# Optimization experiments

Hardware: AMD Instinct MI355X
Metric: run time of the kernel (lower is better)

Reference implementation:

```python
import jax, jax.numpy as jnp
import numpy as np

H = 4            # num_heads
D_HID = 128      # n_hidden (per head)
IN = 256         # in_feats
C = 47           # n_classes
NEG = 0.2        # DGL GATConv default negative_slope
NUM_SRC = (150000, 25000, 6000)
NUM_DST = (25000, 6000, 1024)
NUM_EDGES = (375000, 90000, 10240)


def gat_conv(h_src, h_dst, src, dst, Wsrc, Wdst, al, ar, b, num_dst, out_dim, apply_act):
    # h_src: [Ns, Fin], h_dst: [Nd, Fin]; Wsrc/Wdst: [H*out, Fin]; al/ar: [H, out]; b: [H*out]
    fs = (h_src @ Wsrc.T).reshape(-1, H, out_dim)          # [Ns,H,out]
    fd = (h_dst @ Wdst.T).reshape(-1, H, out_dim)          # [Nd,H,out]
    el = jnp.einsum('nhd,hd->nh', fs, al)                  # [Ns,H]
    er = jnp.einsum('nhd,hd->nh', fd, ar)                  # [Nd,H]
    e = jax.nn.leaky_relu(el[src] + er[dst], NEG)          # [E,H]
    # numerically-stable edge softmax per dst node
    m = jax.ops.segment_max(e, dst, num_segments=num_dst)  # [Nd,H]
    m = jnp.where(jnp.isfinite(m), m, 0.0)                 # guard isolated dst nodes
    ex = jnp.exp(e - m[dst])                               # [E,H]
    s = jax.ops.segment_sum(ex, dst, num_segments=num_dst) # [Nd,H]
    # weighted neighbor aggregation (scatter-add), normalize after the sum
    agg = jax.ops.segment_sum(ex[:, :, None] * fs[src], dst, num_segments=num_dst)  # [Nd,H,out]
    rst = agg / jnp.maximum(s, 1e-9)[:, :, None]
    rst = rst + b.reshape(1, H, out_dim)
    if apply_act:
        rst = jax.nn.elu(rst)
    return rst


def setup_inputs() -> dict:
    key = jax.random.key(0)
    ks = jax.random.split(key, 32)
    inp = {}
    inp['x'] = jax.random.normal(ks[0], (NUM_SRC[0], IN), dtype=jnp.float32)
    # sampled blocks as edge lists (dst nodes are prefix of src nodes)
    inp['src0'] = jax.random.randint(ks[1], (NUM_EDGES[0],), 0, NUM_SRC[0])
    inp['dst0'] = jax.random.randint(ks[2], (NUM_EDGES[0],), 0, NUM_DST[0])
    inp['src1'] = jax.random.randint(ks[3], (NUM_EDGES[1],), 0, NUM_SRC[1])
    inp['dst1'] = jax.random.randint(ks[4], (NUM_EDGES[1],), 0, NUM_DST[1])
    inp['src2'] = jax.random.randint(ks[5], (NUM_EDGES[2],), 0, NUM_SRC[2])
    inp['dst2'] = jax.random.randint(ks[6], (NUM_EDGES[2],), 0, NUM_DST[2])
    # layer params: (in_dim, out_per_head): (256,128), (512,128), (512,47)
    dims = [(IN, D_HID), (H * D_HID, D_HID), (H * D_HID, C)]
    k = 7
    for l, (fin, fout) in enumerate(dims):
        inp[f'Wsrc{l}'] = jax.random.normal(ks[k], (H * fout, fin), dtype=jnp.float32) * 0.05; k += 1
        inp[f'Wdst{l}'] = jax.random.normal(ks[k], (H * fout, fin), dtype=jnp.float32) * 0.05; k += 1
        inp[f'al{l}'] = jax.random.normal(ks[k], (H, fout), dtype=jnp.float32) * 0.05; k += 1
        inp[f'ar{l}'] = jax.random.normal(ks[k], (H, fout), dtype=jnp.float32) * 0.05; k += 1
        inp[f'b{l}'] = jnp.zeros((H * fout,), dtype=jnp.float32); k += 1
    return inp


def reference(x, src0, dst0, src1, dst1, src2, dst2,
              Wsrc0, Wdst0, al0, ar0, b0,
              Wsrc1, Wdst1, al1, ar1, b1,
              Wsrc2, Wdst2, al2, ar2, b2):
    h = x
    # layer 0
    h = gat_conv(h, h[:NUM_DST[0]], src0, dst0, Wsrc0, Wdst0, al0, ar0, b0,
                 NUM_DST[0], D_HID, True).reshape(NUM_DST[0], H * D_HID)
    # layer 1
    h = gat_conv(h, h[:NUM_DST[1]], src1, dst1, Wsrc1, Wdst1, al1, ar1, b1,
                 NUM_DST[1], D_HID, True).reshape(NUM_DST[1], H * D_HID)
    # layer 2 (no activation), mean over heads, log-softmax
    h = gat_conv(h, h[:NUM_DST[2]], src2, dst2, Wsrc2, Wdst2, al2, ar2, b2,
                 NUM_DST[2], C, False)                      # [1024,H,C]
    h = h.mean(axis=1)                                      # [1024,C]
    return jax.nn.log_softmax(h, axis=-1)
```

## Files before the change

kernel.cpp:

```cpp
#include <hip/hip_runtime.h>
#include <math.h>


#define E0 375000
#define E1 90000
#define E2 10240
#define ETOT (E0 + E1 + E2)
#define ND0 25000
#define ND1 6000
#define ND2 1024
#define NTOT (ND0 + ND1 + ND2)
#define NCH ((NTOT + 127) / 128)

static const int L_NS[3]   = {150000, 25000, 6000};
static const int L_ND[3]   = {ND0, ND1, ND2};

typedef short bf8_t __attribute__((ext_vector_type(8)));
typedef float f32x4 __attribute__((ext_vector_type(4)));

__device__ __forceinline__ float lrelu(float v) { return v >= 0.f ? v : 0.2f * v; }
__device__ __forceinline__ unsigned short f2b(float f) {
  unsigned u = __float_as_uint(f);
  unsigned r = u + 0x7fffu + ((u >> 16) & 1u);
  return (unsigned short)(r >> 16);
}
__device__ __forceinline__ float b2f(unsigned v) {
  return __uint_as_float(v << 16);
}
__device__ __forceinline__ unsigned bpack(float a, float b) {
  return (unsigned)f2b(a) | ((unsigned)f2b(b) << 16);
}

__device__ __forceinline__ void gload16(const unsigned short* g, unsigned short* l) {
  __builtin_amdgcn_global_load_lds(
      (const __attribute__((address_space(1))) unsigned int*)g,
      (__attribute__((address_space(3))) unsigned int*)l, 16, 0, 0);
}


__global__ void k_prep_count(
    const int* __restrict__ d0, const int* __restrict__ d1,
    const int* __restrict__ d2, int* __restrict__ cntAll, int* __restrict__ r,
    const float* __restrict__ Ws0, const float* __restrict__ Wd0,
    const float* __restrict__ al0, const float* __restrict__ ar0,
    const float* __restrict__ Ws1, const float* __restrict__ Wd1,
    const float* __restrict__ al1, const float* __restrict__ ar1,
    const float* __restrict__ Ws2, const float* __restrict__ Wd2,
    const float* __restrict__ al2, const float* __restrict__ ar2,
    unsigned short* __restrict__ wlrb, float* __restrict__ wlr1,
    float* __restrict__ wlr2,
    unsigned short* __restrict__ B0, unsigned short* __restrict__ B1,
    unsigned short* __restrict__ B2) {
  const int b = blockIdx.x, t = threadIdx.x;
  int gid = b * 256 + t;
  if (gid < ETOT) {
    int goff, dv;
    if (gid < E0) { goff = 0; dv = d0[gid]; }
    else if (gid < E0 + E1) { goff = ND0; dv = d1[gid - E0]; }
    else { goff = ND0 + ND1; dv = d2[gid - E0 - E1]; }
    r[gid] = atomicAdd(&cntAll[goff + dv], 1);
  }
  if (b < 8) {
    int h = b, hh = h & 3;
    const float* W = (h < 4) ? Ws0 : Wd0;
    const float* a = (h < 4) ? al0 : ar0;
    float acc = 0.f;
    for (int d = 0; d < 128; ++d)
      acc = fmaf(a[hh * 128 + d], W[(size_t)(hh * 128 + d) * 256 + t], acc);
    wlrb[h * 264 + t] = f2b(acc);
  } else if (b == 8) {
    for (int i = t; i < 8 * 264; i += 256) wlrb[8 * 264 + i] = 0;
  } else if (b < 17) {
    int idx = b - 9, which = idx >> 2, h = idx & 3;
    const float* W = which ? Wd1 : Ws1;
    const float* a = which ? ar1 : al1;
#pragma unroll
    for (int kc = 0; kc < 2; ++kc) {
      int k = kc * 256 + t;
      float acc = 0.f;
      for (int d = 0; d < 128; ++d)
        acc = fmaf(a[h * 128 + d], W[(size_t)(h * 128 + d) * 512 + k], acc);
      wlr1[which * 2048 + h * 512 + k] = acc;
    }
  } else if (b < 25) {
    int idx = b - 17, which = idx >> 2, h = idx & 3;
    const float* W = which ? Wd2 : Ws2;
    const float* a = which ? ar2 : al2;
#pragma unroll
    for (int kc = 0; kc < 2; ++kc) {
      int k = kc * 256 + t;
      float acc = 0.f;
      for (int d = 0; d < 47; ++d)
        acc = fmaf(a[h * 47 + d], W[(size_t)(h * 47 + d) * 512 + k], acc);
      wlr2[which * 2048 + h * 512 + k] = acc;
    }
  }
  const int n0 = 512 * 256, n1 = 512 * 512, n2 = 188 * 512;
  for (int i = gid; i < n0 + n1 + n2; i += gridDim.x * 256) {
    if (i < n0) B0[i] = f2b(Ws0[i]);
    else if (i < n0 + n1) B1[i - n0] = f2b(Ws1[i - n0]);
    else B2[i - n0 - n1] = f2b(Ws2[i - n0 - n1]);
  }
}

__global__ __launch_bounds__(128) void k_scanA(const int* __restrict__ cnt,
                                               int* __restrict__ S,
                                               int* __restrict__ btot, int n) {
  __shared__ int wt[2];
  int c = blockIdx.x, t = threadIdx.x, lane = t & 63, w = t >> 6;
  int g = c * 128 + t;
  int v = (g < n) ? cnt[g] : 0;
  int incl = v;
  for (int off = 1; off < 64; off <<= 1) {
    int u = __shfl_up(incl, off);
    if (lane >= off) incl += u;
  }
  if (lane == 63) wt[w] = incl;
  __syncthreads();
  int base = (w == 1) ? wt[0] : 0;
  if (g < n) S[g] = incl - v + base;
  if (t == 127) btot[c] = wt[0] + wt[1];
}

__global__ __launch_bounds__(256) void k_scanB(const int* __restrict__ btot,
                                               int* __restrict__ S, int n, int etot) {
  __shared__ int tv[256];
  int c = blockIdx.x, t = threadIdx.x;
  int own = (t < NCH) ? btot[t] : 0;
  tv[t] = own;
  __syncthreads();
  for (int off = 1; off < 256; off <<= 1) {
    int u = (t >= off) ? tv[t - off] : 0;
    __syncthreads();
    tv[t] += u;
    __syncthreads();
  }
  int base = tv[c] - btot[c];
  int g = c * 128 + (t & 127);
  if (t < 128 && g < n) S[g] += base;
  if (c == 0 && t == 255) S[n] = etot;
}

__global__ void k_scatter_all(
    const int* __restrict__ s0, const int* __restrict__ d0,
    const int* __restrict__ s1, const int* __restrict__ d1,
    const int* __restrict__ s2, const int* __restrict__ d2,
    const int* __restrict__ S, const int* __restrict__ r,
    int* __restrict__ cvAll) {
  int g = blockIdx.x * 256 + threadIdx.x;
  if (g >= ETOT) return;
  int goff, dv, sv;
  if (g < E0) { goff = 0; dv = d0[g]; sv = s0[g]; }
  else if (g < E0 + E1) { int e = g - E0; goff = ND0; dv = d1[e]; sv = s1[e]; }
  else { int e = g - E0 - E1; goff = ND0 + ND1; dv = d2[e]; sv = s2[e]; }
  cvAll[S[goff + dv] + r[g]] = sv;
}


__global__ __launch_bounds__(256) void k_dotc_mfma(
    const float* __restrict__ x, const unsigned short* __restrict__ wlrb,
    float* __restrict__ ell, float* __restrict__ err, int Ns, int Nd) {
  __shared__ unsigned short As[128 * 72];
  __shared__ unsigned short Bs[16 * 264];
  const int tid = threadIdx.x;
  const int w = tid >> 6, lane = tid & 63;
  const int bm = blockIdx.x * 128;
  const int rowg = tid >> 4;
  const int seg  = tid & 15;
  for (int i = tid; i < 16 * 264; i += 256) Bs[i] = wlrb[i];
  f32x4 acc[2] = {};
  for (int k0 = 0; k0 < 256; k0 += 64) {
    __syncthreads();
#pragma unroll
    for (int i = 0; i < 8; ++i) {
      int row = rowg + i * 16;
      int gm = bm + row;
      int gmc = gm < Ns ? gm : Ns - 1;
      float4 a = *reinterpret_cast<const float4*>(x + (size_t)gmc * 256 + k0 + seg * 4);
      ushort4 ub;
      ub.x = f2b(a.x); ub.y = f2b(a.y); ub.z = f2b(a.z); ub.w = f2b(a.w);
      *reinterpret_cast<ushort4*>(&As[row * 72 + seg * 4]) = ub;
    }
    __syncthreads();
    const int ra = w * 32 + (lane & 15);
    const int kf = (lane >> 4) * 8;
#pragma unroll
    for (int ks = 0; ks < 2; ++ks) {
      bf8_t b0 = *reinterpret_cast<const bf8_t*>(&Bs[(lane & 15) * 264 + k0 + ks * 32 + kf]);
      bf8_t a0 = *reinterpret_cast<const bf8_t*>(&As[ra * 72 + ks * 32 + kf]);
      bf8_t a1 = *reinterpret_cast<const bf8_t*>(&As[(ra + 16) * 72 + ks * 32 + kf]);
      acc[0] = __builtin_amdgcn_mfma_f32_16x16x32_bf16(a0, b0, acc[0], 0, 0, 0);
      acc[1] = __builtin_amdgcn_mfma_f32_16x16x32_bf16(a1, b0, acc[1], 0, 0, 0);
    }
  }
  int col = lane & 15;
#pragma unroll
  for (int fm = 0; fm < 2; ++fm) {
#pragma unroll
    for (int j = 0; j < 4; ++j) {
      int node = bm + w * 32 + fm * 16 + (lane >> 4) * 4 + j;
      if (node >= Ns) continue;
      float v = acc[fm][j];
      if (col < 4) ell[(size_t)node * 4 + col] = v;
      else if (col < 8 && node < Nd) err[(size_t)node * 4 + (col - 4)] = v;
    }
  }
}

__device__ __forceinline__ void reduce8_store(float v[8], int lane, int node, int Nd,
                                              float* __restrict__ ell,
                                              float* __restrict__ err) {
#pragma unroll
  for (int h = 0; h < 8; ++h) {
    v[h] += __shfl_xor(v[h], 8);
    v[h] += __shfl_xor(v[h], 16);
    v[h] += __shfl_xor(v[h], 32);
  }
  int sel = lane >> 3;
  float t01 = (sel & 1) ? v[1] : v[0];
  float t23 = (sel & 1) ? v[3] : v[2];
  float t45 = (sel & 1) ? v[5] : v[4];
  float t67 = (sel & 1) ? v[7] : v[6];
  float t03 = (sel & 2) ? t23 : t01;
  float t47 = (sel & 2) ? t67 : t45;
  float s   = (sel & 4) ? t47 : t03;
  s += __shfl_xor(s, 1);
  s += __shfl_xor(s, 2);
  s += __shfl_xor(s, 4);
  if ((lane & 7) == 0) {
    if (sel < 4) ell[(size_t)node * 4 + sel] = s;
    else if (node < Nd) err[(size_t)node * 4 + (sel - 4)] = s;
  }
}

__global__ __launch_bounds__(256) void k_dot_bf(
    const unsigned short* __restrict__ Hs, const float* __restrict__ wlr,
    float* __restrict__ ell, float* __restrict__ err, int Ns, int Nd) {
  int node = blockIdx.x * 4 + (threadIdx.x >> 6);
  int lane = threadIdx.x & 63;
  if (node >= Ns) return;
  uint4 raw = *reinterpret_cast<const uint4*>(Hs + (size_t)node * 512 + lane * 8);
  float xv[8];
  xv[0] = b2f(raw.x & 0xffffu); xv[1] = b2f(raw.x >> 16);
  xv[2] = b2f(raw.y & 0xffffu); xv[3] = b2f(raw.y >> 16);
  xv[4] = b2f(raw.z & 0xffffu); xv[5] = b2f(raw.z >> 16);
  xv[6] = b2f(raw.w & 0xffffu); xv[7] = b2f(raw.w >> 16);
  bool nR = node < Nd;
  float v[8];
#pragma unroll
  for (int h = 0; h < 4; ++h) {
    const float* wp = wlr + h * 512 + lane * 8;
    float4 w0 = *reinterpret_cast<const float4*>(wp);
    float4 w1 = *reinterpret_cast<const float4*>(wp + 4);
    v[h] = xv[0]*w0.x + xv[1]*w0.y + xv[2]*w0.z + xv[3]*w0.w +
           xv[4]*w1.x + xv[5]*w1.y + xv[6]*w1.z + xv[7]*w1.w;
    v[4 + h] = 0.f;
    if (nR) {
      const float* wq = wlr + 2048 + h * 512 + lane * 8;
      float4 u0 = *reinterpret_cast<const float4*>(wq);
      float4 u1 = *reinterpret_cast<const float4*>(wq + 4);
      v[4 + h] = xv[0]*u0.x + xv[1]*u0.y + xv[2]*u0.z + xv[3]*u0.w +
                 xv[4]*u1.x + xv[5]*u1.y + xv[6]*u1.z + xv[7]*u1.w;
    }
  }
  reduce8_store(v, lane, node, Nd, ell, err);
}

template <int FIN, bool F32>
__global__ __launch_bounds__(256) void k_gather4(
    const void* __restrict__ Hv, const float* __restrict__ ell,
    const float* __restrict__ err, const int* __restrict__ rowptr,
    const int* __restrict__ colv, unsigned short* __restrict__ Z, int Nd) {
  constexpr int CPL = F32 ? 4 : 8;
  constexpr int CAP = 256;
  __shared__ float4 esm_all[4][CAP];
  __shared__ int csm_all[4][CAP];
  int w = threadIdx.x >> 6, lane = threadIdx.x & 63;
  int n = blockIdx.x * 4 + w;
  if (n >= Nd) return;
  float4* esm = esm_all[w];
  int* csm = csm_all[w];
  int beg = rowptr[n], cnt = rowptr[n + 1] - beg;
  float4 er4 = *reinterpret_cast<const float4*>(err + (size_t)n * 4);
  float m0 = -INFINITY, m1 = -INFINITY, m2 = -INFINITY, m3 = -INFINITY;
  for (int i = lane; i < cnt; i += 64) {
    int c = colv[beg + i];
    float4 el4 = *reinterpret_cast<const float4*>(ell + (size_t)c * 4);
    float4 e4;
    e4.x = lrelu(el4.x + er4.x); e4.y = lrelu(el4.y + er4.y);
    e4.z = lrelu(el4.z + er4.z); e4.w = lrelu(el4.w + er4.w);
    if (i < CAP) { csm[i] = c; esm[i] = e4; }
    m0 = fmaxf(m0, e4.x); m1 = fmaxf(m1, e4.y);
    m2 = fmaxf(m2, e4.z); m3 = fmaxf(m3, e4.w);
  }
  for (int off = 32; off > 0; off >>= 1) {
    m0 = fmaxf(m0, __shfl_xor(m0, off));
    m1 = fmaxf(m1, __shfl_xor(m1, off));
    m2 = fmaxf(m2, __shfl_xor(m2, off));
    m3 = fmaxf(m3, __shfl_xor(m3, off));
  }
  __builtin_amdgcn_sched_barrier(0);
  float s0 = 0.f, s1 = 0.f, s2 = 0.f, s3 = 0.f;
  float acc[4][CPL] = {};

  auto loadrow = [&](int c, float xv[CPL]) {
    if constexpr (F32) {
      float4 a = *reinterpret_cast<const float4*>(
          (const float*)Hv + (size_t)c * FIN + lane * 4);
      xv[0] = a.x; xv[1] = a.y; xv[2] = a.z; xv[3] = a.w;
    } else {
      uint4 raw = *reinterpret_cast<const uint4*>(
          (const unsigned short*)Hv + (size_t)c * FIN + lane * 8);
      xv[0] = b2f(raw.x & 0xffffu); xv[1] = b2f(raw.x >> 16);
      xv[2] = b2f(raw.y & 0xffffu); xv[3] = b2f(raw.y >> 16);
      xv[4] = b2f(raw.z & 0xffffu); xv[5] = b2f(raw.z >> 16);
      xv[6] = b2f(raw.w & 0xffffu); xv[7] = b2f(raw.w >> 16);
    }
  };
  auto accum = [&](float4 w4, const float xv[CPL]) {
    s0 += w4.x; s1 += w4.y; s2 += w4.z; s3 += w4.w;
#pragma unroll
    for (int c2 = 0; c2 < CPL; ++c2) {
      acc[0][c2] = fmaf(w4.x, xv[c2], acc[0][c2]);
      acc[1][c2] = fmaf(w4.y, xv[c2], acc[1][c2]);
      acc[2][c2] = fmaf(w4.z, xv[c2], acc[2][c2]);
      acc[3][c2] = fmaf(w4.w, xv[c2], acc[3][c2]);
    }
  };

  if (cnt <= CAP) {
    for (int i = lane; i < cnt; i += 64) {
      float4 e = esm[i];
      esm[i] = make_float4(__expf(e.x - m0), __expf(e.y - m1),
                           __expf(e.z - m2), __expf(e.w - m3));
    }
    __builtin_amdgcn_sched_barrier(0);
    int j = 0;
    for (; j + 2 <= cnt; j += 2) {
      int c0 = csm[j], c1 = csm[j + 1];
      float4 wa = esm[j], wb = esm[j + 1];
      float xa[CPL], xb[CPL];
      loadrow(c0, xa);
      loadrow(c1, xb);
      accum(wa, xa);
      accum(wb, xb);
    }
    if (j < cnt) {
      float xa[CPL];
      loadrow(csm[j], xa);
      accum(esm[j], xa);
    }
  } else {
    for (int j = 0; j < cnt; ++j) {
      int c = colv[beg + j];
      float4 el4 = *reinterpret_cast<const float4*>(ell + (size_t)c * 4);
      float4 w4;
      w4.x = __expf(lrelu(el4.x + er4.x) - m0);
      w4.y = __expf(lrelu(el4.y + er4.y) - m1);
      w4.z = __expf(lrelu(el4.z + er4.z) - m2);
      w4.w = __expf(lrelu(el4.w + er4.w) - m3);
      float xa[CPL];
      loadrow(c, xa);
      accum(w4, xa);
    }
  }
  float inv[4];
  inv[0] = 1.f / fmaxf(s0, 1e-9f); inv[1] = 1.f / fmaxf(s1, 1e-9f);
  inv[2] = 1.f / fmaxf(s2, 1e-9f); inv[3] = 1.f / fmaxf(s3, 1e-9f);
#pragma unroll
  for (int h = 0; h < 4; ++h) {
    if constexpr (F32) {
      ushort4 o;
      o.x = f2b(acc[h][0] * inv[h]); o.y = f2b(acc[h][1] * inv[h]);
      o.z = f2b(acc[h][2] * inv[h]); o.w = f2b(acc[h][3] * inv[h]);
      *reinterpret_cast<ushort4*>(Z + (size_t)n * 4 * FIN + h * FIN + lane * 4) = o;
    } else {
      uint4 o;
      o.x = bpack(acc[h][0] * inv[h], acc[h][1] * inv[h]);
      o.y = bpack(acc[h][2] * inv[h], acc[h][3] * inv[h]);
      o.z = bpack(acc[h][4] * inv[h], acc[h][5] * inv[h]);
      o.w = bpack(acc[h][6] * inv[h], acc[h][7] * inv[h]);
      *reinterpret_cast<uint4*>(Z + (size_t)n * 4 * FIN + h * FIN + lane * 8) = o;
    }
  }
}

__global__ __launch_bounds__(256) void k_gemm_l0(
    const unsigned short* __restrict__ Zb, const unsigned short* __restrict__ Wb,
    const float* __restrict__ bias, unsigned short* __restrict__ out, int M) {
  __shared__ unsigned short Bs[4 * 128 * 64];
  const int tid = threadIdx.x;
  const int w = tid >> 6, lane = tid & 63;
  const int h = blockIdx.z;
  const int bm = blockIdx.x * 128;
  const unsigned short* Ag = Zb + (size_t)h * 256;
  const unsigned short* Bg = Wb + (size_t)h * 128 * 256;
  const int lrow = lane >> 3;
  const int gseg = (lane & 7) ^ lrow;
#pragma unroll
  for (int i = 0; i < 16; ++i) {
    int cidx = w * 16 + i;
    int kb = cidx >> 4, ch = cidx & 15;
    int row = ch * 8 + lrow;
    gload16(Bg + (size_t)row * 256 + kb * 64 + gseg * 8, Bs + kb * 8192 + ch * 512);
  }
  __syncthreads();

  f32x4 acc[2][8];
#pragma unroll
  for (int i = 0; i < 2; ++i)
#pragma unroll
    for (int j = 0; j < 8; ++j) acc[i][j] = (f32x4){0.f, 0.f, 0.f, 0.f};

  const int colsel = lane >> 4;
  int rowA = bm + w * 32 + (lane & 15);
  int gm0 = rowA < M ? rowA : M - 1;
  int gm1 = (rowA + 16) < M ? (rowA + 16) : M - 1;
#pragma unroll
  for (int step = 0; step < 8; ++step) {
    int kb = step >> 1, ks = step & 1;
    int kcol = kb * 64 + ks * 32 + colsel * 8;
    bf8_t a0 = *reinterpret_cast<const bf8_t*>(Ag + (size_t)gm0 * 1024 + kcol);
    bf8_t a1 = *reinterpret_cast<const bf8_t*>(Ag + (size_t)gm1 * 1024 + kcol);
    int cs = ((((ks << 2) + colsel) ^ (lane & 7)) << 3);
#pragma unroll
    for (int fn = 0; fn < 8; ++fn) {
      bf8_t bf = *reinterpret_cast<const bf8_t*>(
          Bs + kb * 8192 + (fn * 16 + (lane & 15)) * 64 + cs);
      acc[0][fn] = __builtin_amdgcn_mfma_f32_16x16x32_bf16(a0, bf, acc[0][fn], 0, 0, 0);
      acc[1][fn] = __builtin_amdgcn_mfma_f32_16x16x32_bf16(a1, bf, acc[1][fn], 0, 0, 0);
    }
  }
#pragma unroll
  for (int fm = 0; fm < 2; ++fm) {
#pragma unroll
    for (int fn = 0; fn < 8; ++fn) {
      int colb = fn * 16 + (lane & 15);
      float bv = bias[h * 128 + colb];
#pragma unroll
      for (int j = 0; j < 4; ++j) {
        int rowb = bm + w * 32 + fm * 16 + (lane >> 4) * 4 + j;
        if (rowb >= M) continue;
        float v = acc[fm][fn][j] + bv;
        v = v > 0.f ? v : (__expf(v) - 1.f);
        out[(size_t)rowb * 512 + h * 128 + colb] = f2b(v);
      }
    }
  }
}

template <int BN, bool ACT, bool OUTBF>
__global__ __launch_bounds__(256) void k_gemm_mfma(
    const unsigned short* __restrict__ Zb, const unsigned short* __restrict__ Wb,
    const float* __restrict__ bias, void* __restrict__ outv,
    int M, int N, int K) {
  constexpr int FN = BN / 16;
  constexpr int AI = 4;
  constexpr int BI = BN / 32;
  int h = blockIdx.z;
  __shared__ unsigned short As[128 * 64];
  __shared__ unsigned short Bs[BN * 64];
  const int tid = threadIdx.x;
  const int w = tid >> 6, lane = tid & 63;
  const int bm = blockIdx.x * 128, bn = blockIdx.y * BN;
  const int lda = 4 * K;
  const unsigned short* Ag = Zb + (size_t)h * K;
  const unsigned short* Bg = Wb + (size_t)h * N * K;
  const int lrow = lane >> 3;
  const int gseg = (lane & 7) ^ lrow;
  f32x4 acc[2][FN];
#pragma unroll
  for (int i = 0; i < 2; ++i)
#pragma unroll
    for (int j = 0; j < FN; ++j) acc[i][j] = (f32x4){0.f, 0.f, 0.f, 0.f};

  for (int k0 = 0; k0 < K; k0 += 64) {
    __syncthreads();
#pragma unroll
    for (int i = 0; i < AI; ++i) {
      int ch = w * AI + i;
      int row = ch * 8 + lrow;
      int gm = bm + row; gm = gm < M ? gm : M - 1;
      gload16(Ag + (size_t)gm * lda + k0 + gseg * 8, As + ch * 512);
    }
#pragma unroll
    for (int i = 0; i < BI; ++i) {
      int ch = w * BI + i;
      int row = ch * 8 + lrow;
      int gn = bn + row; gn = gn < N ? gn : N - 1;
      gload16(Bg + (size_t)gn * K + k0 + gseg * 8, Bs + ch * 512);
    }
    __syncthreads();
    const int ra = w * 32 + (lane & 15);
#pragma unroll
    for (int ks = 0; ks < 2; ++ks) {
      int cs = ((((ks << 2) + (lane >> 4)) ^ (lane & 7)) << 3);
      bf8_t a0 = *reinterpret_cast<const bf8_t*>(As + ra * 64 + cs);
      bf8_t a1 = *reinterpret_cast<const bf8_t*>(As + (ra + 16) * 64 + cs);
#pragma unroll
      for (int fn = 0; fn < FN; ++fn) {
        bf8_t bf = *reinterpret_cast<const bf8_t*>(Bs + (fn * 16 + (lane & 15)) * 64 + cs);
        acc[0][fn] = __builtin_amdgcn_mfma_f32_16x16x32_bf16(a0, bf, acc[0][fn], 0, 0, 0);
        acc[1][fn] = __builtin_amdgcn_mfma_f32_16x16x32_bf16(a1, bf, acc[1][fn], 0, 0, 0);
      }
    }
  }
  int ldo = 4 * N;
#pragma unroll
  for (int fm = 0; fm < 2; ++fm) {
#pragma unroll
    for (int fn = 0; fn < FN; ++fn) {
      int colb = bn + fn * 16 + (lane & 15);
      if (colb >= N) continue;
      float bv = bias[h * N + colb];
#pragma unroll
      for (int j = 0; j < 4; ++j) {
        int rowb = bm + w * 32 + fm * 16 + (lane >> 4) * 4 + j;
        if (rowb >= M) continue;
        float v = acc[fm][fn][j] + bv;
        if (ACT) v = v > 0.f ? v : (__expf(v) - 1.f);
        size_t off = (size_t)rowb * ldo + (size_t)h * N + colb;
        if (OUTBF) ((unsigned short*)outv)[off] = f2b(v);
        else ((float*)outv)[off] = v;
      }
    }
  }
}

__global__ __launch_bounds__(256) void k_mean_lsm(const float* __restrict__ rst2,
                                                  float* __restrict__ out, int Nd) {
  int node = blockIdx.x * 4 + (threadIdx.x >> 6);
  int lane = threadIdx.x & 63;
  if (node >= Nd) return;
  const float* r = rst2 + (size_t)node * 188;
  float vv = 0.f;
  if (lane < 47)
    vv = 0.25f * (r[lane] + r[47 + lane] + r[94 + lane] + r[141 + lane]);
  float m = (lane < 47) ? vv : -INFINITY;
  for (int off = 32; off > 0; off >>= 1) m = fmaxf(m, __shfl_xor(m, off));
  float ex = (lane < 47) ? __expf(vv - m) : 0.f;
  float ss = ex;
  for (int off = 32; off > 0; off >>= 1) ss += __shfl_xor(ss, off);
  if (lane < 47) out[(size_t)node * 47 + lane] = vv - m - logf(ss);
}

extern "C" void kernel_launch(void* const* d_in, const int* in_sizes, int n_in,
                              void* d_out, int out_size, void* d_ws, size_t ws_size,
                              hipStream_t stream) {
  (void)in_sizes; (void)n_in; (void)out_size; (void)ws_size;
  const float* x = (const float*)d_in[0];
  const int* srcs[3] = {(const int*)d_in[1], (const int*)d_in[3], (const int*)d_in[5]};
  const int* dsts[3] = {(const int*)d_in[2], (const int*)d_in[4], (const int*)d_in[6]};
  const float* Wsrc[3] = {(const float*)d_in[7], (const float*)d_in[12], (const float*)d_in[17]};
  const float* Wdst[3] = {(const float*)d_in[8], (const float*)d_in[13], (const float*)d_in[18]};
  const float* al[3]   = {(const float*)d_in[9], (const float*)d_in[14], (const float*)d_in[19]};
  const float* ar[3]   = {(const float*)d_in[10], (const float*)d_in[15], (const float*)d_in[20]};
  const float* bb[3]   = {(const float*)d_in[11], (const float*)d_in[16], (const float*)d_in[21]};

  char* p = (char*)d_ws;
  auto alloc = [&](size_t bytes) -> void* {
    void* r = (void*)p;
    p += (bytes + 255) & ~(size_t)255;
    return r;
  };
  unsigned short* zbf = (unsigned short*)alloc((size_t)25000 * 1024 * 2);
  unsigned short* h1  = (unsigned short*)alloc((size_t)25000 * 512 * 2);
  unsigned short* h2  = (unsigned short*)alloc((size_t)6000 * 512 * 2);
  float* rst2   = (float*)alloc((size_t)1024 * 188 * 4);
  unsigned short* Wb0 = (unsigned short*)alloc((size_t)512 * 256 * 2);
  unsigned short* Wb1 = (unsigned short*)alloc((size_t)512 * 512 * 2);
  unsigned short* Wb2 = (unsigned short*)alloc((size_t)188 * 512 * 2);
  float* ell    = (float*)alloc((size_t)150000 * 4 * 4);
  float* err    = (float*)alloc((size_t)25000 * 4 * 4);
  int* cntAll   = (int*)alloc((size_t)NTOT * 4);
  int* Sarr     = (int*)alloc((size_t)(NTOT + 8) * 4);
  int* btot     = (int*)alloc((size_t)((NCH + 7) & ~7) * 4);
  int* r_all    = (int*)alloc((size_t)ETOT * 4);
  int* cvAll    = (int*)alloc((size_t)ETOT * 4);
  unsigned short* wlrb = (unsigned short*)alloc((size_t)16 * 264 * 2);
  float* wlr1   = (float*)alloc((size_t)8 * 512 * 4);
  float* wlr2   = (float*)alloc((size_t)8 * 512 * 4);

  hipMemsetAsync(cntAll, 0, (size_t)NTOT * 4, stream);
  k_prep_count<<<(ETOT + 255) / 256, 256, 0, stream>>>(
      dsts[0], dsts[1], dsts[2], cntAll, r_all,
      Wsrc[0], Wdst[0], al[0], ar[0], Wsrc[1], Wdst[1], al[1], ar[1],
      Wsrc[2], Wdst[2], al[2], ar[2], wlrb, wlr1, wlr2, Wb0, Wb1, Wb2);
  k_scanA<<<NCH, 128, 0, stream>>>(cntAll, Sarr, btot, NTOT);
  k_scanB<<<NCH, 256, 0, stream>>>(btot, Sarr, NTOT, ETOT);
  k_scatter_all<<<(ETOT + 255) / 256, 256, 0, stream>>>(
      srcs[0], dsts[0], srcs[1], dsts[1], srcs[2], dsts[2], Sarr, r_all, cvAll);

  const unsigned short* Hbf[3] = {nullptr, h1, h2};
  const unsigned short* Wbf[3] = {Wb0, Wb1, Wb2};
  const float* wlrs[3] = {nullptr, wlr1, wlr2};
  const int noff[3] = {0, ND0, ND0 + ND1};

  for (int l = 0; l < 3; ++l) {
    int Ns = L_NS[l], Nd = L_ND[l];
    if (l == 0) {
      k_dotc_mfma<<<(Ns + 127) / 128, 256, 0, stream>>>(x, wlrb, ell, err, Ns, Nd);
      k_gather4<256, true><<<(Nd + 3) / 4, 256, 0, stream>>>(
          x, ell, err, Sarr + noff[l], cvAll, zbf, Nd);
    } else {
      k_dot_bf<<<(Ns + 3) / 4, 256, 0, stream>>>(Hbf[l], wlrs[l], ell, err, Ns, Nd);
      k_gather4<512, false><<<(Nd + 3) / 4, 256, 0, stream>>>(
          Hbf[l], ell, err, Sarr + noff[l], cvAll, zbf, Nd);
    }
    if (l == 0) {
      dim3 g((Nd + 127) / 128, 1, 4);
      k_gemm_l0<<<g, 256, 0, stream>>>(zbf, Wbf[l], bb[l], h1, Nd);
    } else if (l == 1) {
      dim3 g((Nd + 127) / 128, 1, 4);
      k_gemm_mfma<128, true, true><<<g, 256, 0, stream>>>(zbf, Wbf[l], bb[l], h2, Nd, 128, 512);
    } else {
      dim3 g((Nd + 127) / 128, 1, 4);
      k_gemm_mfma<64, false, false><<<g, 256, 0, stream>>>(zbf, Wbf[l], bb[l], rst2, Nd, 47, 512);
    }
  }
  k_mean_lsm<<<(1024 + 3) / 4, 256, 0, stream>>>(rst2, (float*)d_out, 1024);
}
```

Before: 253.8 us.

## Load A fragments directly from global in dotc and add specialized layer-1 GEMM

The layer-0 attention-dot kernel now reads x rows straight from global memory into MFMA A fragments, converting to bf16 in registers. This removes the LDS staging and the per-k-tile barriers. A new k_gemm_l1 kernel replaces the generic templated GEMM for layer 1: it stages half of the per-head weight matrix at a time in a swizzled LDS buffer, with only two syncs, and reads A fragments directly from global. The risks are less coalesced global reads of A and a larger LDS footprint (64KB), which may lower occupancy.

```diff
diff --git a/kernel.cpp b/kernel.cpp
--- a/kernel.cpp
+++ b/kernel.cpp
@@ -160,38 +160,39 @@
 __global__ __launch_bounds__(256) void k_dotc_mfma(
     const float* __restrict__ x, const unsigned short* __restrict__ wlrb,
     float* __restrict__ ell, float* __restrict__ err, int Ns, int Nd) {
-  __shared__ unsigned short As[128 * 72];
   __shared__ unsigned short Bs[16 * 264];
   const int tid = threadIdx.x;
   const int w = tid >> 6, lane = tid & 63;
   const int bm = blockIdx.x * 128;
-  const int rowg = tid >> 4;
-  const int seg  = tid & 15;
   for (int i = tid; i < 16 * 264; i += 256) Bs[i] = wlrb[i];
+  __syncthreads();
+  const int kf = (lane >> 4) * 8;
+  int rowA = bm + w * 32 + (lane & 15);
+  int gm0 = rowA < Ns ? rowA : Ns - 1;
+  int gm1 = (rowA + 16) < Ns ? (rowA + 16) : Ns - 1;
+  const float* a0p = x + (size_t)gm0 * 256;
+  const float* a1p = x + (size_t)gm1 * 256;
+  const unsigned short* bp = &Bs[(lane & 15) * 264];
   f32x4 acc[2] = {};
-  for (int k0 = 0; k0 < 256; k0 += 64) {
-    __syncthreads();
-#pragma unroll
-    for (int i = 0; i < 8; ++i) {
-      int row = rowg + i * 16;
-      int gm = bm + row;
-      int gmc = gm < Ns ? gm : Ns - 1;
-      float4 a = *reinterpret_cast<const float4*>(x + (size_t)gmc * 256 + k0 + seg * 4);
-      ushort4 ub;
-      ub.x = f2b(a.x); ub.y = f2b(a.y); ub.z = f2b(a.z); ub.w = f2b(a.w);
-      *reinterpret_cast<ushort4*>(&As[row * 72 + seg * 4]) = ub;
-    }
-    __syncthreads();
-    const int ra = w * 32 + (lane & 15);
-    const int kf = (lane >> 4) * 8;
-#pragma unroll
-    for (int ks = 0; ks < 2; ++ks) {
-      bf8_t b0 = *reinterpret_cast<const bf8_t*>(&Bs[(lane & 15) * 264 + k0 + ks * 32 + kf]);
-      bf8_t a0 = *reinterpret_cast<const bf8_t*>(&As[ra * 72 + ks * 32 + kf]);
-      bf8_t a1 = *reinterpret_cast<const bf8_t*>(&As[(ra + 16) * 72 + ks * 32 + kf]);
-      acc[0] = __builtin_amdgcn_mfma_f32_16x16x32_bf16(a0, b0, acc[0], 0, 0, 0);
-      acc[1] = __builtin_amdgcn_mfma_f32_16x16x32_bf16(a1, b0, acc[1], 0, 0, 0);
-    }
+#pragma unroll
+  for (int step = 0; step < 8; ++step) {
+    int col = (step >> 1) * 64 + (step & 1) * 32 + kf;
+    float4 f0a = *reinterpret_cast<const float4*>(a0p + col);
+    float4 f0b = *reinterpret_cast<const float4*>(a0p + col + 4);
+    float4 f1a = *reinterpret_cast<const float4*>(a1p + col);
+    float4 f1b = *reinterpret_cast<const float4*>(a1p + col + 4);
+    bf8_t a0, a1;
+    a0[0] = (short)f2b(f0a.x); a0[1] = (short)f2b(f0a.y);
+    a0[2] = (short)f2b(f0a.z); a0[3] = (short)f2b(f0a.w);
+    a0[4] = (short)f2b(f0b.x); a0[5] = (short)f2b(f0b.y);
+    a0[6] = (short)f2b(f0b.z); a0[7] = (short)f2b(f0b.w);
+    a1[0] = (short)f2b(f1a.x); a1[1] = (short)f2b(f1a.y);
+    a1[2] = (short)f2b(f1a.z); a1[3] = (short)f2b(f1a.w);
+    a1[4] = (short)f2b(f1b.x); a1[5] = (short)f2b(f1b.y);
+    a1[6] = (short)f2b(f1b.z); a1[7] = (short)f2b(f1b.w);
+    bf8_t b0 = *reinterpret_cast<const bf8_t*>(bp + col);
+    acc[0] = __builtin_amdgcn_mfma_f32_16x16x32_bf16(a0, b0, acc[0], 0, 0, 0);
+    acc[1] = __builtin_amdgcn_mfma_f32_16x16x32_bf16(a1, b0, acc[1], 0, 0, 0);
   }
   int col = lane & 15;
 #pragma unroll
@@ -449,6 +450,75 @@
   }
 }
 
+__global__ __launch_bounds__(256) void k_gemm_l1(
+    const unsigned short* __restrict__ Zb, const unsigned short* __restrict__ Wb,
+    const float* __restrict__ bias, unsigned short* __restrict__ out, int M) {
+  __shared__ unsigned short Bs[4 * 128 * 64];
+  const int tid = threadIdx.x;
+  const int w = tid >> 6, lane = tid & 63;
+  const int h = blockIdx.z;
+  const int bm = blockIdx.x * 128;
+  const unsigned short* Ag = Zb + (size_t)h * 512;
+  const unsigned short* Bg = Wb + (size_t)h * 128 * 512;
+  const int lrow = lane >> 3;
+  const int gseg = (lane & 7) ^ lrow;
+  const int colsel = lane >> 4;
+  int rowA = bm + w * 32 + (lane & 15);
+  int gm0 = rowA < M ? rowA : M - 1;
+  int gm1 = (rowA + 16) < M ? (rowA + 16) : M - 1;
+
+  f32x4 acc[2][8];
+#pragma unroll
+  for (int i = 0; i < 2; ++i)
+#pragma unroll
+    for (int j = 0; j < 8; ++j) acc[i][j] = (f32x4){0.f, 0.f, 0.f, 0.f};
+
+#pragma unroll
+  for (int half = 0; half < 2; ++half) {
+    if (half) __syncthreads();
+#pragma unroll
+    for (int i = 0; i < 16; ++i) {
+      int cidx = w * 16 + i;
+      int kb = cidx >> 4, ch = cidx & 15;
+      int row = ch * 8 + lrow;
+      gload16(Bg + (size_t)row * 512 + half * 256 + kb * 64 + gseg * 8,
+              Bs + kb * 8192 + ch * 512);
+    }
+    __syncthreads();
+#pragma unroll
+    for (int step = 0; step < 8; ++step) {
+      int kb = step >> 1, ks = step & 1;
+      int kcol = half * 256 + kb * 64 + ks * 32 + colsel * 8;
+      bf8_t a0 = *reinterpret_cast<const bf8_t*>(Ag + (size_t)gm0 * 2048 + kcol);
+      bf8_t a1 = *reinterpret_cast<const bf8_t*>(Ag + (size_t)gm1 * 2048 + kcol);
+      int cs = ((((ks << 2) + colsel) ^ (lane & 7)) << 3);
+#pragma unroll
+      for (int fn = 0; fn < 8; ++fn) {
+        bf8_t bf = *reinterpret_cast<const bf8_t*>(
+            Bs + kb * 8192 + (fn * 16 + (lane & 15)) * 64 + cs);
+        acc[0][fn] = __builtin_amdgcn_mfma_f32_16x16x32_bf16(a0, bf, acc[0][fn], 0, 0, 0);
+        acc[1][fn] = __builtin_amdgcn_mfma_f32_16x16x32_bf16(a1, bf, acc[1][fn], 0, 0, 0);
+      }
+    }
+  }
+#pragma unroll
+  for (int fm = 0; fm < 2; ++fm) {
+#pragma unroll
+    for (int fn = 0; fn < 8; ++fn) {
+      int colb = fn * 16 + (lane & 15);
+      float bv = bias[h * 128 + colb];
+#pragma unroll
+      for (int j = 0; j < 4; ++j) {
+        int rowb = bm + w * 32 + fm * 16 + (lane >> 4) * 4 + j;
+        if (rowb >= M) continue;
+        float v = acc[fm][fn][j] + bv;
+        v = v > 0.f ? v : (__expf(v) - 1.f);
+        out[(size_t)rowb * 512 + h * 128 + colb] = f2b(v);
+      }
+    }
+  }
+}
+
 template <int BN, bool ACT, bool OUTBF>
 __global__ __launch_bounds__(256) void k_gemm_mfma(
     const unsigned short* __restrict__ Zb, const unsigned short* __restrict__ Wb,
@@ -612,7 +682,7 @@
       k_gemm_l0<<<g, 256, 0, stream>>>(zbf, Wbf[l], bb[l], h1, Nd);
     } else if (l == 1) {
       dim3 g((Nd + 127) / 128, 1, 4);
-      k_gemm_mfma<128, true, true><<<g, 256, 0, stream>>>(zbf, Wbf[l], bb[l], h2, Nd, 128, 512);
+      k_gemm_l1<<<g, 256, 0, stream>>>(zbf, Wbf[l], bb[l], h2, Nd);
     } else {
       dim3 g((Nd + 127) / 128, 1, 4);
       k_gemm_mfma<64, false, false><<<g, 256, 0, stream>>>(zbf, Wbf[l], bb[l], rst2, Nd, 47, 512);
```

After: 251.9 us. About the same (-0.7%).
